# Kernel tuning notes

Hardware: AMD Instinct MI355X
Metric: run time of the kernel (lower is better)

## Reference

```python
import jax, jax.numpy as jnp
import numpy as np

N, D, H, C, K, L = 50000, 256, 128, 40, 4, 2
E = 800000


def setup_inputs() -> dict:
    key = jax.random.key(0)
    ks = jax.random.split(key, 20)
    g = lambda k, s: jax.random.normal(k, s, dtype=jnp.float32) * 0.05
    z = lambda s: jnp.zeros(s, dtype=jnp.float32)
    return {
        "x": jax.random.normal(ks[0], (N, D), dtype=jnp.float32),
        "edge_index": jax.random.randint(ks[1], (2, E), 0, N, dtype=jnp.int32),
        "fc0_w": g(ks[2], (D, H)), "fc0_b": z((H,)),
        "fc1_w": g(ks[3], (H, C)), "fc1_b": z((C,)),
        "env_w": g(ks[4], (L, H, K)), "env_b": z((L, K)),
        "conv_w": g(ks[5], (L, K, 2 * H, H)),
        "q_w": g(ks[6], (H, H)), "q_b": z((H,)),
        "k_w": g(ks[7], (H, H)), "k_b": z((H,)),
        "v_w": g(ks[8], (H, H)), "v_b": z((H,)),
        "envp_w": g(ks[9], (H, K)), "envp_b": z((K,)),
        "genv_w": g(ks[10], (K, H, H)),
        "gt_w": g(ks[11], (H, H)), "gt_b": z((H,)),
    }


def _gcn_conv(h, row, col, n):
    # symmetric normalization using in-degree array (deg computed from col, as in source)
    deg = jax.ops.segment_sum(jnp.ones_like(col, dtype=h.dtype), col, num_segments=n)
    inv = jnp.where(deg > 0, 1.0 / jnp.sqrt(deg), 0.0)
    val = inv[col] * inv[row]                      # [E]
    msg = val[:, None] * h[row]                    # [E, H] gather
    return jax.ops.segment_sum(msg, col, num_segments=n)  # scatter to dst


def _canet_conv(h, row, col, env, w):
    # sum_k e_k [W_D^k * A_norm h ; W_S^k * h] via cat + per-env GEMM, residual
    hi = jnp.concatenate([_gcn_conv(h, row, col, h.shape[0]), h], axis=1)  # [N, 2H]
    out_k = jnp.einsum('nd,kdh->nkh', hi, w)       # [N, K, H]
    return jnp.einsum('nk,nkh->nh', env, out_k) + h


def _linear_transformer(h, q_w, q_b, k_w, k_b, v_w, v_b, envp_w, envp_b):
    n = h.shape[0]
    q = h @ q_w + q_b
    k = h @ k_w + k_b
    v = h @ v_w + v_b
    q = q / jnp.maximum(jnp.linalg.norm(q), 1e-12)  # fro-norm of whole matrix
    k = k / jnp.maximum(jnp.linalg.norm(k), 1e-12)
    ksum = jnp.sum(k, axis=0)                       # k^T @ ones -> [H]
    attn_norm = 1.0 + (q @ ksum)[:, None] / n       # [N,1]
    gr = (v + q @ (k.T @ v) / n) / jnp.maximum(attn_norm, 1e-12)
    return gr, gr @ envp_w + envp_b


def _forward(x, edge_index, fc0_w, fc0_b, fc1_w, fc1_b, env_w, env_b, conv_w,
             q_w, q_b, k_w, k_b, v_w, v_b, envp_w, envp_b, genv_w, gt_w, gt_b):
    row, col = edge_index[0], edge_index[1]
    h = jax.nn.relu(x @ fc0_w + fc0_b)
    for i in range(L):
        logits = h @ env_w[i] + env_b[i]            # node env encoder
        env = jax.nn.softmax(logits, axis=-1)       # eval-mode sampling
        h = jax.nn.relu(_canet_conv(h, row, col, env, conv_w[i]))
    local_logits = h @ fc1_w + fc1_b                # [N, C]
    gr, glog = _linear_transformer(h, q_w, q_b, k_w, k_b, v_w, v_b, envp_w, envp_b)
    genv = jax.nn.softmax(glog, axis=-1)            # [N, K]
    gpe = jnp.einsum('nh,khe->nke', gr, genv_w)     # per-env global transforms
    ctx = jnp.einsum('nk,nkh->nh', genv, gpe)
    gh = jax.nn.relu(ctx @ gt_w + gt_b)
    global_logits = gh @ fc1_w + fc1_b
    return 0.5 * (local_logits + global_logits)     # fused prediction


def reference(x, edge_index, fc0_w, fc0_b, fc1_w, fc1_b, env_w, env_b, conv_w,
              q_w, q_b, k_w, k_b, v_w, v_b, envp_w, envp_b, genv_w, gt_w, gt_b):
    return _forward(x, edge_index, fc0_w, fc0_b, fc1_w, fc1_b, env_w, env_b, conv_w,
                    q_w, q_b, k_w, k_b, v_w, v_b, envp_w, envp_b, genv_w, gt_w, gt_b)
```

## Files before the change

kernel.cpp:

```cpp
#include <hip/hip_runtime.h>

#define DEV __device__ __forceinline__

static constexpr int NN = 50000;
static constexpr int DD = 256;
static constexpr int HH = 128;
static constexpr int CC = 40;
static constexpr int KK = 4;
static constexpr int EE = 800000;
static constexpr int MP = 50176;
static constexpr int SKV = 196;
static constexpr int CPB = 8;
static constexpr int CSB = 391;

typedef __attribute__((ext_vector_type(8))) short bf16x8;
typedef __attribute__((ext_vector_type(4))) float f32x4;

DEV unsigned short f2bf(float f) {
  union { float f; unsigned int i; } c; c.f = f;
  unsigned int x = c.i;
  x += 0x7FFFu + ((x >> 16) & 1u);
  return (unsigned short)(x >> 16);
}
DEV float bfbits2f(unsigned int hi16bits) {
  union { unsigned int i; float f; } c; c.i = hi16bits; return c.f;
}

__global__ void MLEI_12970801234193_kernel(float* out, int n) {
  int i = blockIdx.x * blockDim.x + threadIdx.x;
  if (i < n) out[i] = 7.0f;
}

__global__ void zero_i32_kernel(int* p, int n) {
  int i = blockIdx.x * blockDim.x + threadIdx.x;
  if (i < n) p[i] = 0;
}

__global__ void padzero_kernel(unsigned short* kT, unsigned short* vT) {
  int i = blockIdx.x * blockDim.x + threadIdx.x;
  const int PW = MP - NN;
  if (i >= HH * PW) return;
  int f = i / PW, c = i - f * PW;
  kT[(size_t)f * MP + NN + c] = 0;
  vT[(size_t)f * MP + NN + c] = 0;
}

__global__ void tcvt_kernel(const float* __restrict__ src, unsigned short* __restrict__ dst,
                            int K, int N, int nm) {
  int i = blockIdx.x * blockDim.x + threadIdx.x;
  int tot = nm * K * N;
  if (i >= tot) return;
  int m = i / (K * N);
  int rem = i - m * K * N;
  int k = rem / N;
  int n = rem - k * N;
  dst[(size_t)m * K * N + (size_t)n * K + k] = f2bf(src[i]);
}

__global__ __launch_bounds__(256) void mgemm_kernel(
    const float* __restrict__ A, const float* __restrict__ Aadd, int lda,
    const unsigned short* __restrict__ Bt, int K,
    int emode, float* __restrict__ out, int ldo,
    const float* __restrict__ bias, const float* __restrict__ resid, int ldr,
    const float* __restrict__ anorm, const float* __restrict__ red,
    unsigned short* __restrict__ outT,
    unsigned short* __restrict__ outBf, const float* __restrict__ rowscale,
    int M, int Nd) {
  __shared__ unsigned short As[2][128][40];
  __shared__ unsigned short Bs[2][128][40];
  const int tid = threadIdx.x, lane = tid & 63, wave = tid >> 6;
  const int quad = lane >> 4, l16 = lane & 15;
  const int wm = (wave >> 1) * 64, wn = (wave & 1) * 64;
  const int bm = blockIdx.x * 128;
  const int srow = tid >> 1, skh = (tid & 1) * 16;
  const int grow = bm + srow;
  const bool rowok = grow < M;
  const bool colok = srow < Nd;
  const int NCH = K >> 5;

  f32x4 acc[4][4];
#pragma unroll
  for (int i = 0; i < 4; ++i)
#pragma unroll
    for (int j = 0; j < 4; ++j)
#pragma unroll
      for (int r = 0; r < 4; ++r) acc[i][j][r] = 0.f;

  float va[16];
  bf16x8 b0, b1;

  auto LOAD = [&](int kc) {
    int k0 = kc << 5;
    if (rowok) {
      const float* ap = A + (size_t)grow * lda + k0 + skh;
      float4 v0 = *(const float4*)(ap + 0), v1 = *(const float4*)(ap + 4);
      float4 v2 = *(const float4*)(ap + 8), v3 = *(const float4*)(ap + 12);
      va[0] = v0.x; va[1] = v0.y; va[2] = v0.z; va[3] = v0.w;
      va[4] = v1.x; va[5] = v1.y; va[6] = v1.z; va[7] = v1.w;
      va[8] = v2.x; va[9] = v2.y; va[10] = v2.z; va[11] = v2.w;
      va[12] = v3.x; va[13] = v3.y; va[14] = v3.z; va[15] = v3.w;
      if (Aadd) {
        const float* ap2 = Aadd + (size_t)grow * lda + k0 + skh;
        float4 w0 = *(const float4*)(ap2 + 0), w1 = *(const float4*)(ap2 + 4);
        float4 w2 = *(const float4*)(ap2 + 8), w3 = *(const float4*)(ap2 + 12);
        va[0] += w0.x; va[1] += w0.y; va[2] += w0.z; va[3] += w0.w;
        va[4] += w1.x; va[5] += w1.y; va[6] += w1.z; va[7] += w1.w;
        va[8] += w2.x; va[9] += w2.y; va[10] += w2.z; va[11] += w2.w;
        va[12] += w3.x; va[13] += w3.y; va[14] += w3.z; va[15] += w3.w;
      }
    }
    if (colok) {
      const unsigned short* bp = Bt + (size_t)srow * K + k0 + skh;
      b0 = *(const bf16x8*)(bp);
      b1 = *(const bf16x8*)(bp + 8);
    } else {
#pragma unroll
      for (int z = 0; z < 8; ++z) { b0[z] = 0; b1[z] = 0; }
    }
  };

  auto STORE = [&](int buf) {
    bf16x8 p0, p1;
    if (rowok) {
#pragma unroll
      for (int z = 0; z < 8; ++z) { p0[z] = (short)f2bf(va[z]); p1[z] = (short)f2bf(va[z + 8]); }
    } else {
#pragma unroll
      for (int z = 0; z < 8; ++z) { p0[z] = 0; p1[z] = 0; }
    }
    *(bf16x8*)&As[buf][srow][skh] = p0;
    *(bf16x8*)&As[buf][srow][skh + 8] = p1;
    *(bf16x8*)&Bs[buf][srow][skh] = b0;
    *(bf16x8*)&Bs[buf][srow][skh + 8] = b1;
  };

  LOAD(0);
  STORE(0);
  __syncthreads();

  for (int kc = 0; kc < NCH; ++kc) {
    const int cur = kc & 1;
    const bool more = (kc + 1) < NCH;
    if (more) LOAD(kc + 1);
    bf16x8 af[4], bfr[4];
#pragma unroll
    for (int i = 0; i < 4; ++i) af[i] = *(const bf16x8*)&As[cur][wm + i * 16 + l16][quad * 8];
#pragma unroll
    for (int j = 0; j < 4; ++j) bfr[j] = *(const bf16x8*)&Bs[cur][wn + j * 16 + l16][quad * 8];
#pragma unroll
    for (int i = 0; i < 4; ++i)
#pragma unroll
      for (int j = 0; j < 4; ++j)
        acc[i][j] = __builtin_amdgcn_mfma_f32_16x16x32_bf16(af[i], bfr[j], acc[i][j], 0, 0, 0);
    if (more) STORE(cur ^ 1);
    __syncthreads();
  }

  float s2 = (emode == 3) ? red[2] : 0.f;
#pragma unroll
  for (int j = 0; j < 4; ++j) {
    int col = wn + j * 16 + l16;
    if (col >= Nd) continue;
    float bv = bias ? bias[col] : 0.f;
#pragma unroll
    for (int i = 0; i < 4; ++i) {
      int row0 = bm + wm + i * 16 + quad * 4;
      if (row0 >= M) continue;
      float o[4];
#pragma unroll
      for (int r = 0; r < 4; ++r) {
        float a = acc[i][j][r];
        int row = row0 + r;
        if (emode == 0) o[r] = a + bv;
        else if (emode == 1) o[r] = fmaxf(a + bv, 0.f);
        else if (emode == 3) o[r] = (resid[(size_t)row * ldr + col] + a * s2) / anorm[row];
        else o[r] = 0.5f * a + bv;
        out[(size_t)row * ldo + col] = o[r];
      }
      if (outT) {
        ushort4 pk;
        pk.x = f2bf(o[0]); pk.y = f2bf(o[1]); pk.z = f2bf(o[2]); pk.w = f2bf(o[3]);
        *(ushort4*)&outT[(size_t)col * MP + row0] = pk;
      }
      if (outBf) {
#pragma unroll
        for (int r = 0; r < 4; ++r) {
          float rs = rowscale ? rowscale[row0 + r] : 1.f;
          outBf[(size_t)(row0 + r) * 128 + col] = f2bf(o[r] * rs);
        }
      }
    }
  }
}

__global__ __launch_bounds__(256) void ktv_mfma_kernel(
    const unsigned short* __restrict__ kT, const unsigned short* __restrict__ vT,
    float* __restrict__ part) {
  __shared__ unsigned short As[2][128][40];
  __shared__ unsigned short Bs[2][128][40];
  const int tid = threadIdx.x, lane = tid & 63, wave = tid >> 6;
  const int quad = lane >> 4, l16 = lane & 15;
  const int wm = (wave >> 1) * 64, wn = (wave & 1) * 64;
  const int srow = tid >> 1, skh = (tid & 1) * 16;

  f32x4 acc[4][4];
#pragma unroll
  for (int i = 0; i < 4; ++i)
#pragma unroll
    for (int j = 0; j < 4; ++j)
#pragma unroll
      for (int r = 0; r < 4; ++r) acc[i][j][r] = 0.f;

  const int nb0 = blockIdx.x * (CPB * 32);
  bf16x8 k0, k1, v0, v1;

  auto LOAD = [&](int c) {
    int nb = nb0 + c * 32;
    const unsigned short* kp = kT + (size_t)srow * MP + nb + skh;
    k0 = *(const bf16x8*)(kp);
    k1 = *(const bf16x8*)(kp + 8);
    const unsigned short* vp = vT + (size_t)srow * MP + nb + skh;
    v0 = *(const bf16x8*)(vp);
    v1 = *(const bf16x8*)(vp + 8);
  };
  auto STORE = [&](int buf) {
    *(bf16x8*)&As[buf][srow][skh] = k0;
    *(bf16x8*)&As[buf][srow][skh + 8] = k1;
    *(bf16x8*)&Bs[buf][srow][skh] = v0;
    *(bf16x8*)&Bs[buf][srow][skh + 8] = v1;
  };

  LOAD(0);
  STORE(0);
  __syncthreads();

  for (int c = 0; c < CPB; ++c) {
    const int cur = c & 1;
    const bool more = (c + 1) < CPB;
    if (more) LOAD(c + 1);
    bf16x8 af[4], bfr[4];
#pragma unroll
    for (int i = 0; i < 4; ++i) af[i] = *(const bf16x8*)&As[cur][wm + i * 16 + l16][quad * 8];
#pragma unroll
    for (int j = 0; j < 4; ++j) bfr[j] = *(const bf16x8*)&Bs[cur][wn + j * 16 + l16][quad * 8];
#pragma unroll
    for (int i = 0; i < 4; ++i)
#pragma unroll
      for (int j = 0; j < 4; ++j)
        acc[i][j] = __builtin_amdgcn_mfma_f32_16x16x32_bf16(af[i], bfr[j], acc[i][j], 0, 0, 0);
    if (more) STORE(cur ^ 1);
    __syncthreads();
  }

  float* pb = part + (size_t)blockIdx.x * 16384;
#pragma unroll
  for (int j = 0; j < 4; ++j) {
    int col = wn + j * 16 + l16;
#pragma unroll
    for (int i = 0; i < 4; ++i) {
      int row0 = wm + i * 16 + quad * 4;
      *(f32x4*)&pb[col * 128 + row0] = acc[i][j];
    }
  }
}

__global__ void ktv_reduce_kernel(const float* __restrict__ part,
                                  unsigned short* __restrict__ Btktv) {
  int i = blockIdx.x * blockDim.x + threadIdx.x;
  if (i >= 16384) return;
  float s = 0.f;
  for (int b = 0; b < SKV; ++b) s += part[(size_t)b * 16384 + i];
  Btktv[i] = f2bf(s);
}

__global__ __launch_bounds__(256) void mconv_kernel(
    const float* __restrict__ A1, const float* __restrict__ A2,
    const float* __restrict__ env, const unsigned short* __restrict__ Btc, int Kpe,
    int relu_resid, const float* __restrict__ resid, float* __restrict__ out,
    unsigned short* __restrict__ outBf, const float* __restrict__ rowscale, int M) {
  __shared__ unsigned short As[2][128][40];
  __shared__ unsigned short Bs[2][128][40];
  __shared__ float envs[4][128];
  const int tid = threadIdx.x, lane = tid & 63, wave = tid >> 6;
  const int quad = lane >> 4, l16 = lane & 15;
  const int wm = (wave >> 1) * 64, wn = (wave & 1) * 64;
  const int bm = blockIdx.x * 128;
  const int srow = tid >> 1, skh = (tid & 1) * 16;
  const int grow = bm + srow;
  const bool rowok = grow < M;

  for (int i = tid; i < 512; i += 256) {
    int r = i >> 2, c = i & 3;
    int g = bm + r;
    envs[c][r] = (g < M) ? env[(size_t)g * 4 + c] : 0.f;
  }
  __syncthreads();

  const int npe = Kpe >> 5;
  const int lg = (npe == 8) ? 3 : 2;
  const int NCH = npe << 2;

  f32x4 acc[4][4];
#pragma unroll
  for (int i = 0; i < 4; ++i)
#pragma unroll
    for (int j = 0; j < 4; ++j)
#pragma unroll
      for (int r = 0; r < 4; ++r) acc[i][j][r] = 0.f;

  float4 v0, v1, v2, v3;
  bf16x8 b0, b1;
  float ev = 0.f;

  auto LOAD = [&](int kc) {
    int e = kc >> lg;
    int kof = (kc & (npe - 1)) << 5;
    ev = envs[e][srow];
    const float* Asrc = A1;
    int ks = kof;
    if (A2 && kof >= 128) { Asrc = A2; ks = kof - 128; }
    if (rowok) {
      const float* ap = Asrc + (size_t)grow * 128 + ks + skh;
      v0 = *(const float4*)(ap + 0);
      v1 = *(const float4*)(ap + 4);
      v2 = *(const float4*)(ap + 8);
      v3 = *(const float4*)(ap + 12);
    }
    const unsigned short* bp = Btc + ((size_t)e * 128 + srow) * Kpe + kof + skh;
    b0 = *(const bf16x8*)(bp);
    b1 = *(const bf16x8*)(bp + 8);
  };

  auto STORE = [&](int buf) {
    bf16x8 p0, p1;
    if (rowok) {
      p0[0] = (short)f2bf(v0.x * ev); p0[1] = (short)f2bf(v0.y * ev);
      p0[2] = (short)f2bf(v0.z * ev); p0[3] = (short)f2bf(v0.w * ev);
      p0[4] = (short)f2bf(v1.x * ev); p0[5] = (short)f2bf(v1.y * ev);
      p0[6] = (short)f2bf(v1.z * ev); p0[7] = (short)f2bf(v1.w * ev);
      p1[0] = (short)f2bf(v2.x * ev); p1[1] = (short)f2bf(v2.y * ev);
      p1[2] = (short)f2bf(v2.z * ev); p1[3] = (short)f2bf(v2.w * ev);
      p1[4] = (short)f2bf(v3.x * ev); p1[5] = (short)f2bf(v3.y * ev);
      p1[6] = (short)f2bf(v3.z * ev); p1[7] = (short)f2bf(v3.w * ev);
    } else {
#pragma unroll
      for (int z = 0; z < 8; ++z) { p0[z] = 0; p1[z] = 0; }
    }
    *(bf16x8*)&As[buf][srow][skh] = p0;
    *(bf16x8*)&As[buf][srow][skh + 8] = p1;
    *(bf16x8*)&Bs[buf][srow][skh] = b0;
    *(bf16x8*)&Bs[buf][srow][skh + 8] = b1;
  };

  LOAD(0);
  STORE(0);
  __syncthreads();

  for (int kc = 0; kc < NCH; ++kc) {
    const int cur = kc & 1;
    const bool more = (kc + 1) < NCH;
    if (more) LOAD(kc + 1);
    bf16x8 af[4], bfr[4];
#pragma unroll
    for (int i = 0; i < 4; ++i) af[i] = *(const bf16x8*)&As[cur][wm + i * 16 + l16][quad * 8];
#pragma unroll
    for (int j = 0; j < 4; ++j) bfr[j] = *(const bf16x8*)&Bs[cur][wn + j * 16 + l16][quad * 8];
#pragma unroll
    for (int i = 0; i < 4; ++i)
#pragma unroll
      for (int j = 0; j < 4; ++j)
        acc[i][j] = __builtin_amdgcn_mfma_f32_16x16x32_bf16(af[i], bfr[j], acc[i][j], 0, 0, 0);
    if (more) STORE(cur ^ 1);
    __syncthreads();
  }

#pragma unroll
  for (int j = 0; j < 4; ++j) {
    int col = wn + j * 16 + l16;
#pragma unroll
    for (int i = 0; i < 4; ++i) {
      int row0 = bm + wm + i * 16 + quad * 4;
      if (row0 >= M) continue;
#pragma unroll
      for (int r = 0; r < 4; ++r) {
        int row = row0 + r;
        float a = acc[i][j][r];
        float o = relu_resid ? fmaxf(a + resid[(size_t)row * 128 + col], 0.f) : a;
        out[(size_t)row * 128 + col] = o;
        if (outBf) {
          float rs = rowscale ? rowscale[row] : 1.f;
          outBf[(size_t)row * 128 + col] = f2bf(o * rs);
        }
      }
    }
  }
}

__global__ void count_kernel(const int* ei, int* deg, int E) {
  int e = blockIdx.x * blockDim.x + threadIdx.x;
  if (e >= E) return;
  atomicAdd(&deg[ei[E + e]], 1);
}

__global__ __launch_bounds__(128) void scan1_kernel(const int* __restrict__ deg,
                                                    int* __restrict__ bsum, int n) {
  __shared__ int sh[128];
  int t = threadIdx.x;
  int i = blockIdx.x * 128 + t;
  sh[t] = (i < n) ? deg[i] : 0;
  __syncthreads();
  for (int off = 64; off > 0; off >>= 1) {
    if (t < off) sh[t] += sh[t + off];
    __syncthreads();
  }
  if (t == 0) bsum[blockIdx.x] = sh[0];
}

__global__ __launch_bounds__(512) void scan2_kernel(const int* __restrict__ bsum,
                                                    int* __restrict__ boff, int nb,
                                                    int* __restrict__ startN) {
  __shared__ int sh[512];
  int t = threadIdx.x;
  int v0 = (t < nb) ? bsum[t] : 0;
  sh[t] = v0;
  __syncthreads();
  for (int off = 1; off < 512; off <<= 1) {
    int v = sh[t];
    int add = (t >= off) ? sh[t - off] : 0;
    __syncthreads();
    sh[t] = v + add;
    __syncthreads();
  }
  if (t < nb) boff[t] = sh[t] - v0;
  if (t == nb - 1) *startN = sh[t];
}

__global__ __launch_bounds__(128) void scan3_kernel(const int* __restrict__ deg,
                                                    const int* __restrict__ boff,
                                                    int* __restrict__ start,
                                                    int* __restrict__ cursor,
                                                    float* __restrict__ inv, int n) {
  __shared__ int sh[128];
  int t = threadIdx.x;
  int i = blockIdx.x * 128 + t;
  int d = (i < n) ? deg[i] : 0;
  sh[t] = d;
  __syncthreads();
  for (int off = 1; off < 128; off <<= 1) {
    int v = sh[t];
    int add = (t >= off) ? sh[t - off] : 0;
    __syncthreads();
    sh[t] = v + add;
    __syncthreads();
  }
  if (i < n) {
    int p = boff[blockIdx.x] + sh[t] - d;
    start[i] = p; cursor[i] = p;
    inv[i] = (d > 0) ? rsqrtf((float)d) : 0.f;
  }
}

__global__ void fill_kernel(const int* ei, int* cursor, int* bucket, int E) {
  int e = blockIdx.x * blockDim.x + threadIdx.x;
  if (e >= E) return;
  int r = ei[e], c = ei[E + e];
  int pos = atomicAdd(&cursor[c], 1);
  bucket[pos] = r;
}

__global__ __launch_bounds__(256) void gather_kernel(
    const unsigned short* __restrict__ hs, const int* __restrict__ start,
    const int* __restrict__ bucket, const float* __restrict__ inv,
    float* __restrict__ agg, int n) {
  int node = blockIdx.x * 4 + (threadIdx.x >> 6);
  if (node >= n) return;
  const int lane = threadIdx.x & 63;
  const int half = lane >> 5, l32 = lane & 31;
  const int f4 = l32 * 4;
  int s0 = start[node], s1 = start[node + 1];
  float a0 = 0.f, a1 = 0.f, a2 = 0.f, a3 = 0.f;
  int j = s0 + half;
  for (; j + 2 < s1; j += 4) {
    int r0 = bucket[j], r1 = bucket[j + 2];
    uint2 u0 = *(const uint2*)&hs[(size_t)r0 * 128 + f4];
    uint2 u1 = *(const uint2*)&hs[(size_t)r1 * 128 + f4];
    a0 += bfbits2f(u0.x << 16); a1 += bfbits2f(u0.x & 0xFFFF0000u);
    a2 += bfbits2f(u0.y << 16); a3 += bfbits2f(u0.y & 0xFFFF0000u);
    a0 += bfbits2f(u1.x << 16); a1 += bfbits2f(u1.x & 0xFFFF0000u);
    a2 += bfbits2f(u1.y << 16); a3 += bfbits2f(u1.y & 0xFFFF0000u);
  }
  for (; j < s1; j += 2) {
    int r = bucket[j];
    uint2 u = *(const uint2*)&hs[(size_t)r * 128 + f4];
    a0 += bfbits2f(u.x << 16); a1 += bfbits2f(u.x & 0xFFFF0000u);
    a2 += bfbits2f(u.y << 16); a3 += bfbits2f(u.y & 0xFFFF0000u);
  }
  a0 += __shfl_xor(a0, 32);
  a1 += __shfl_xor(a1, 32);
  a2 += __shfl_xor(a2, 32);
  a3 += __shfl_xor(a3, 32);
  if (half == 0) {
    float iv = inv[node];
    *(float4*)&agg[(size_t)node * 128 + f4] = make_float4(iv * a0, iv * a1, iv * a2, iv * a3);
  }
}

__global__ __launch_bounds__(256) void env_softmax_kernel(const float* __restrict__ h,
                                                          const float* __restrict__ w,
                                                          const float* __restrict__ b,
                                                          float* __restrict__ env, int M) {
  __shared__ float hsd[64][129];
  __shared__ float ws[HH * KK];
  int tid = threadIdx.x;
  int base = blockIdx.x * 64;
  for (int i = tid; i < HH * KK; i += 256) ws[i] = w[i];
  {
    int row = tid >> 2, q4 = (tid & 3) * 32;
    int g = base + row;
    if (g < M) {
      const float* hp = h + (size_t)g * HH + q4;
#pragma unroll
      for (int z = 0; z < 8; ++z) {
        float4 v = *(const float4*)(hp + z * 4);
        hsd[row][q4 + z * 4 + 0] = v.x; hsd[row][q4 + z * 4 + 1] = v.y;
        hsd[row][q4 + z * 4 + 2] = v.z; hsd[row][q4 + z * 4 + 3] = v.w;
      }
    }
  }
  __syncthreads();
  if (tid < 64 && base + tid < M) {
    float l0 = b[0], l1 = b[1], l2 = b[2], l3 = b[3];
    for (int d = 0; d < HH; ++d) {
      float hv = hsd[tid][d];
      l0 += hv * ws[d * 4 + 0]; l1 += hv * ws[d * 4 + 1];
      l2 += hv * ws[d * 4 + 2]; l3 += hv * ws[d * 4 + 3];
    }
    float m = fmaxf(fmaxf(l0, l1), fmaxf(l2, l3));
    float e0 = __expf(l0 - m), e1 = __expf(l1 - m), e2 = __expf(l2 - m), e3 = __expf(l3 - m);
    float s = 1.f / (e0 + e1 + e2 + e3);
    *(float4*)(env + (size_t)(base + tid) * KK) = make_float4(e0 * s, e1 * s, e2 * s, e3 * s);
  }
}

__global__ __launch_bounds__(256) void colstats1_kernel(
    const float* __restrict__ q, const float* __restrict__ k,
    float* __restrict__ partK, float* __restrict__ partS, int n) {
  int tid = threadIdx.x, ty = tid >> 7, tx = tid & 127;
  int lo = blockIdx.x * 128 + ty, hi = min(n, blockIdx.x * 128 + 128);
  float ks = 0.f, sq = 0.f, sk = 0.f;
  for (int r = lo; r < hi; r += 2) {
    float kv = k[(size_t)r * HH + tx];
    float qv = q[(size_t)r * HH + tx];
    ks += kv; sq += qv * qv; sk += kv * kv;
  }
  __shared__ float sks[2][128];
  __shared__ float ssq[256], ssk[256];
  sks[ty][tx] = ks; ssq[tid] = sq; ssk[tid] = sk;
  __syncthreads();
  if (ty == 0) partK[(size_t)blockIdx.x * 128 + tx] = sks[0][tx] + sks[1][tx];
  for (int off = 128; off > 0; off >>= 1) {
    if (tid < off) { ssq[tid] += ssq[tid + off]; ssk[tid] += ssk[tid + off]; }
    __syncthreads();
  }
  if (tid == 0) { partS[blockIdx.x * 2] = ssq[0]; partS[blockIdx.x * 2 + 1] = ssk[0]; }
}

__global__ __launch_bounds__(256) void colstats2_kernel(
    const float* __restrict__ partK, const float* __restrict__ partS,
    float* __restrict__ ksum, float* __restrict__ red) {
  int t = threadIdx.x;
  if (t < 128) {
    float s = 0.f;
    for (int b = 0; b < CSB; ++b) s += partK[(size_t)b * 128 + t];
    ksum[t] = s;
  } else if (t == 128 || t == 129) {
    float s = 0.f;
    for (int b = 0; b < CSB; ++b) s += partS[b * 2 + (t - 128)];
    red[t - 128] = s;
  }
}

__global__ void scale_kernel(float* red, int n) {
  float nq = fmaxf(sqrtf(red[0]), 1e-12f);
  float nk = fmaxf(sqrtf(red[1]), 1e-12f);
  red[2] = 1.f / (nq * nk * (float)n);
}

__global__ __launch_bounds__(256) void anorm_kernel(const float* q, const float* ksum,
                                                    const float* red, float* anorm, int M) {
  __shared__ float ks[HH];
  for (int i = threadIdx.x; i < HH; i += blockDim.x) ks[i] = ksum[i];
  __syncthreads();
  int n = blockIdx.x * blockDim.x + threadIdx.x;
  if (n >= M) return;
  const float* qp = q + (size_t)n * HH;
  float d = 0.f;
  for (int i = 0; i < HH; ++i) d += qp[i] * ks[i];
  float a = 1.f + d * red[2];
  anorm[n] = fmaxf(a, 1e-12f);
}

extern "C" void kernel_launch(void* const* d_in, const int* in_sizes, int n_in,
                              void* d_out, int out_size, void* d_ws, size_t ws_size,
                              hipStream_t stream) {
  const float* x = (const float*)d_in[0];
  const int* ei = (const int*)d_in[1];
  const float* fc0_w = (const float*)d_in[2];
  const float* fc0_b = (const float*)d_in[3];
  const float* fc1_w = (const float*)d_in[4];
  const float* fc1_b = (const float*)d_in[5];
  const float* env_w = (const float*)d_in[6];
  const float* env_b = (const float*)d_in[7];
  const float* conv_w = (const float*)d_in[8];
  const float* q_w = (const float*)d_in[9];
  const float* q_b = (const float*)d_in[10];
  const float* k_w = (const float*)d_in[11];
  const float* k_b = (const float*)d_in[12];
  const float* v_w = (const float*)d_in[13];
  const float* v_b = (const float*)d_in[14];
  const float* envp_w = (const float*)d_in[15];
  const float* envp_b = (const float*)d_in[16];
  const float* genv_w = (const float*)d_in[17];
  const float* gt_w = (const float*)d_in[18];
  const float* gt_b = (const float*)d_in[19];
  float* out = (float*)d_out;

  const size_t NH = (size_t)NN * HH;
  float* W = (float*)d_ws;
  float* hA = W;
  float* hB = W + NH;
  float* agg = W + 2 * NH;
  float* vbuf = W + 3 * NH;
  float* gr = W + 4 * NH;
  float* env = W + 5 * NH;
  float* genv = env + (size_t)NN * KK;
  float* inv = genv + (size_t)NN * KK;
  float* anorm = inv + NN;
  float* ksum = anorm + NN;
  float* red = ksum + HH;
  int* deg = (int*)(red + 4);
  int* start = deg + NN;
  int* cursor = start + NN + 1;
  int* bucket = cursor + NN;
  int* bsum = bucket + EE;
  int* boff = bsum + CSB;
  unsigned short* wb = (unsigned short*)(((uintptr_t)(boff + CSB) + 15) & ~(uintptr_t)15);
  unsigned short* Btfc0 = wb;
  unsigned short* Btq = Btfc0 + 32768;
  unsigned short* Btk = Btq + 16384;
  unsigned short* Btv = Btk + 16384;
  unsigned short* Btgt = Btv + 16384;
  unsigned short* Btfc1 = Btgt + 16384;
  unsigned short* Btconv = Btfc1 + 5120;
  unsigned short* Btgenv = Btconv + 262144;
  unsigned short* Btktv = Btgenv + 65536;
  unsigned short* kTbf = Btktv + 16384;
  unsigned short* vTbf = kTbf + (size_t)HH * MP;
  unsigned short* hsb = vTbf + (size_t)HH * MP;
  float* part = (float*)(((uintptr_t)(hsb + NH) + 15) & ~(uintptr_t)15);
  float* partK = part + (size_t)SKV * 16384;
  float* partS = partK + (size_t)CSB * 128;

  float* q = agg;
  float* kb = hB;
  float* ctx = hB;
  float* gh = vbuf;

  dim3 b256(256);
  const int MB = (NN + 127) / 128;

  zero_i32_kernel<<<dim3((NN + 255) / 256), b256, 0, stream>>>(deg, NN);
  padzero_kernel<<<dim3((HH * (MP - NN) + 255) / 256), b256, 0, stream>>>(kTbf, vTbf);

  count_kernel<<<dim3((EE + 255) / 256), b256, 0, stream>>>(ei, deg, EE);
  scan1_kernel<<<dim3(CSB), dim3(128), 0, stream>>>(deg, bsum, NN);
  scan2_kernel<<<dim3(1), dim3(512), 0, stream>>>(bsum, boff, CSB, start + NN);
  scan3_kernel<<<dim3(CSB), dim3(128), 0, stream>>>(deg, boff, start, cursor, inv, NN);
  fill_kernel<<<dim3((EE + 255) / 256), b256, 0, stream>>>(ei, cursor, bucket, EE);

  tcvt_kernel<<<dim3((32768 + 255) / 256), b256, 0, stream>>>(fc0_w, Btfc0, 256, 128, 1);
  tcvt_kernel<<<dim3((16384 + 255) / 256), b256, 0, stream>>>(q_w, Btq, 128, 128, 1);
  tcvt_kernel<<<dim3((16384 + 255) / 256), b256, 0, stream>>>(k_w, Btk, 128, 128, 1);
  tcvt_kernel<<<dim3((16384 + 255) / 256), b256, 0, stream>>>(v_w, Btv, 128, 128, 1);
  tcvt_kernel<<<dim3((16384 + 255) / 256), b256, 0, stream>>>(gt_w, Btgt, 128, 128, 1);
  tcvt_kernel<<<dim3((5120 + 255) / 256), b256, 0, stream>>>(fc1_w, Btfc1, 128, 40, 1);
  tcvt_kernel<<<dim3((262144 + 255) / 256), b256, 0, stream>>>(conv_w, Btconv, 256, 128, 8);
  tcvt_kernel<<<dim3((65536 + 255) / 256), b256, 0, stream>>>(genv_w, Btgenv, 128, 128, 4);

  mgemm_kernel<<<dim3(MB), b256, 0, stream>>>(
      x, nullptr, DD, Btfc0, 256, 1, hA, HH, fc0_b, nullptr, 0, nullptr, nullptr,
      nullptr, hsb, inv, NN, HH);

  float* hcur = hA;
  float* hnext = hB;
  for (int l = 0; l < 2; ++l) {
    env_softmax_kernel<<<dim3((NN + 63) / 64), b256, 0, stream>>>(
        hcur, env_w + (size_t)l * HH * KK, env_b + (size_t)l * KK, env, NN);
    gather_kernel<<<dim3(NN / 4), b256, 0, stream>>>(hsb, start, bucket, inv, agg, NN);
    mconv_kernel<<<dim3(MB), b256, 0, stream>>>(
        agg, hcur, env, Btconv + (size_t)l * 131072, 256, 1, hcur, hnext,
        (l == 0) ? hsb : nullptr, inv, NN);
    float* t = hcur; hcur = hnext; hnext = t;
  }

  mgemm_kernel<<<dim3(MB), b256, 0, stream>>>(
      hcur, nullptr, HH, Btq, 128, 0, q, HH, q_b, nullptr, 0, nullptr, nullptr,
      nullptr, nullptr, nullptr, NN, HH);
  mgemm_kernel<<<dim3(MB), b256, 0, stream>>>(
      hcur, nullptr, HH, Btk, 128, 0, kb, HH, k_b, nullptr, 0, nullptr, nullptr,
      kTbf, nullptr, nullptr, NN, HH);
  mgemm_kernel<<<dim3(MB), b256, 0, stream>>>(
      hcur, nullptr, HH, Btv, 128, 0, vbuf, HH, v_b, nullptr, 0, nullptr, nullptr,
      vTbf, nullptr, nullptr, NN, HH);

  colstats1_kernel<<<dim3(CSB), b256, 0, stream>>>(q, kb, partK, partS, NN);
  colstats2_kernel<<<dim3(1), b256, 0, stream>>>(partK, partS, ksum, red);
  ktv_mfma_kernel<<<dim3(SKV), b256, 0, stream>>>(kTbf, vTbf, part);
  ktv_reduce_kernel<<<dim3(64), b256, 0, stream>>>(part, Btktv);
  scale_kernel<<<dim3(1), dim3(1), 0, stream>>>(red, NN);
  anorm_kernel<<<dim3((NN + 255) / 256), b256, 0, stream>>>(q, ksum, red, anorm, NN);

  mgemm_kernel<<<dim3(MB), b256, 0, stream>>>(
      q, nullptr, HH, Btktv, 128, 3, gr, HH, nullptr, vbuf, HH, anorm, red,
      nullptr, nullptr, nullptr, NN, HH);

  env_softmax_kernel<<<dim3((NN + 63) / 64), b256, 0, stream>>>(gr, envp_w, envp_b, genv, NN);

  mconv_kernel<<<dim3(MB), b256, 0, stream>>>(
      gr, nullptr, genv, Btgenv, 128, 0, nullptr, ctx, nullptr, nullptr, NN);

  mgemm_kernel<<<dim3(MB), b256, 0, stream>>>(
      ctx, nullptr, HH, Btgt, 128, 1, gh, HH, gt_b, nullptr, 0, nullptr, nullptr,
      nullptr, nullptr, nullptr, NN, HH);

  mgemm_kernel<<<dim3(MB), b256, 0, stream>>>(
      hcur, gh, HH, Btfc1, 128, 5, out, CC, fc1_b, nullptr, 0, nullptr, nullptr,
      nullptr, nullptr, nullptr, NN, CC);
}
```

Baseline: 700.9 us.

## Deepen GEMM prefetch to two chunks and reorder mconv loop for A reuse

The generic GEMM and the k^T v partial kernel now keep two register sets of prefetched operands, so each global load is issued two k-chunks ahead of its MFMA use. The mconv kernel reads its env weights straight into registers instead of staging them through shared memory with an extra barrier. It also reorders its loop so each A chunk is loaded once and reused across all four env weight slices, rather than reloaded for every env. The cost is higher register pressure, which may lower occupancy, and more complex loop control.

Measured after the change: 688.6 us. Within noise of the previous version (-1.8%).

```diff
diff --git a/kernel.cpp b/kernel.cpp
--- a/kernel.cpp
+++ b/kernel.cpp
@@ -86,10 +86,10 @@
 #pragma unroll
       for (int r = 0; r < 4; ++r) acc[i][j][r] = 0.f;
 
-  float va[16];
-  bf16x8 b0, b1;
-
-  auto LOAD = [&](int kc) {
+  float vaA[16], vaB[16];
+  bf16x8 bA0, bA1, bB0, bB1;
+
+  auto LOAD = [&](int kc, float (&va)[16], bf16x8& b0, bf16x8& b1) {
     int k0 = kc << 5;
     if (rowok) {
       const float* ap = A + (size_t)grow * lda + k0 + skh;
@@ -119,7 +119,7 @@
     }
   };
 
-  auto STORE = [&](int buf) {
+  auto STORE = [&](int buf, const float (&va)[16], const bf16x8& b0, const bf16x8& b1) {
     bf16x8 p0, p1;
     if (rowok) {
 #pragma unroll
@@ -134,26 +134,35 @@
     *(bf16x8*)&Bs[buf][srow][skh + 8] = b1;
   };
 
-  LOAD(0);
-  STORE(0);
-  __syncthreads();
-
-  for (int kc = 0; kc < NCH; ++kc) {
-    const int cur = kc & 1;
-    const bool more = (kc + 1) < NCH;
-    if (more) LOAD(kc + 1);
+  auto MFMA = [&](int buf) {
     bf16x8 af[4], bfr[4];
 #pragma unroll
-    for (int i = 0; i < 4; ++i) af[i] = *(const bf16x8*)&As[cur][wm + i * 16 + l16][quad * 8];
-#pragma unroll
-    for (int j = 0; j < 4; ++j) bfr[j] = *(const bf16x8*)&Bs[cur][wn + j * 16 + l16][quad * 8];
+    for (int i = 0; i < 4; ++i) af[i] = *(const bf16x8*)&As[buf][wm + i * 16 + l16][quad * 8];
+#pragma unroll
+    for (int j = 0; j < 4; ++j) bfr[j] = *(const bf16x8*)&Bs[buf][wn + j * 16 + l16][quad * 8];
 #pragma unroll
     for (int i = 0; i < 4; ++i)
 #pragma unroll
       for (int j = 0; j < 4; ++j)
         acc[i][j] = __builtin_amdgcn_mfma_f32_16x16x32_bf16(af[i], bfr[j], acc[i][j], 0, 0, 0);
-    if (more) STORE(cur ^ 1);
+  };
+
+  LOAD(0, vaA, bA0, bA1);
+  if (NCH > 1) LOAD(1, vaB, bB0, bB1);
+  STORE(0, vaA, bA0, bA1);
+  __syncthreads();
+
+  for (int kc = 0; kc < NCH; kc += 2) {
+    if (kc + 2 < NCH) LOAD(kc + 2, vaA, bA0, bA1);
+    MFMA(0);
+    if (kc + 1 < NCH) STORE(1, vaB, bB0, bB1);
     __syncthreads();
+    if (kc + 1 < NCH) {
+      if (kc + 3 < NCH) LOAD(kc + 3, vaB, bB0, bB1);
+      MFMA(1);
+      if (kc + 2 < NCH) STORE(0, vaA, bA0, bA1);
+      __syncthreads();
+    }
   }
 
   float s2 = (emode == 3) ? red[2] : 0.f;
@@ -212,9 +221,9 @@
       for (int r = 0; r < 4; ++r) acc[i][j][r] = 0.f;
 
   const int nb0 = blockIdx.x * (CPB * 32);
-  bf16x8 k0, k1, v0, v1;
-
-  auto LOAD = [&](int c) {
+  bf16x8 kA0, kA1, vA0, vA1, kB0, kB1, vB0, vB1;
+
+  auto LOAD = [&](int c, bf16x8& k0, bf16x8& k1, bf16x8& v0, bf16x8& v1) {
     int nb = nb0 + c * 32;
     const unsigned short* kp = kT + (size_t)srow * MP + nb + skh;
     k0 = *(const bf16x8*)(kp);
@@ -223,33 +232,41 @@
     v0 = *(const bf16x8*)(vp);
     v1 = *(const bf16x8*)(vp + 8);
   };
-  auto STORE = [&](int buf) {
+  auto STORE = [&](int buf, const bf16x8& k0, const bf16x8& k1, const bf16x8& v0, const bf16x8& v1) {
     *(bf16x8*)&As[buf][srow][skh] = k0;
     *(bf16x8*)&As[buf][srow][skh + 8] = k1;
     *(bf16x8*)&Bs[buf][srow][skh] = v0;
     *(bf16x8*)&Bs[buf][srow][skh + 8] = v1;
   };
-
-  LOAD(0);
-  STORE(0);
-  __syncthreads();
-
-  for (int c = 0; c < CPB; ++c) {
-    const int cur = c & 1;
-    const bool more = (c + 1) < CPB;
-    if (more) LOAD(c + 1);
+  auto MFMA = [&](int buf) {
     bf16x8 af[4], bfr[4];
 #pragma unroll
-    for (int i = 0; i < 4; ++i) af[i] = *(const bf16x8*)&As[cur][wm + i * 16 + l16][quad * 8];
-#pragma unroll
-    for (int j = 0; j < 4; ++j) bfr[j] = *(const bf16x8*)&Bs[cur][wn + j * 16 + l16][quad * 8];
+    for (int i = 0; i < 4; ++i) af[i] = *(const bf16x8*)&As[buf][wm + i * 16 + l16][quad * 8];
+#pragma unroll
+    for (int j = 0; j < 4; ++j) bfr[j] = *(const bf16x8*)&Bs[buf][wn + j * 16 + l16][quad * 8];
 #pragma unroll
     for (int i = 0; i < 4; ++i)
 #pragma unroll
       for (int j = 0; j < 4; ++j)
         acc[i][j] = __builtin_amdgcn_mfma_f32_16x16x32_bf16(af[i], bfr[j], acc[i][j], 0, 0, 0);
-    if (more) STORE(cur ^ 1);
+  };
+
+  LOAD(0, kA0, kA1, vA0, vA1);
+  LOAD(1, kB0, kB1, vB0, vB1);
+  STORE(0, kA0, kA1, vA0, vA1);
+  __syncthreads();
+
+  for (int c = 0; c < CPB; c += 2) {
+    if (c + 2 < CPB) LOAD(c + 2, kA0, kA1, vA0, vA1);
+    MFMA(0);
+    if (c + 1 < CPB) STORE(1, kB0, kB1, vB0, vB1);
     __syncthreads();
+    if (c + 1 < CPB) {
+      if (c + 3 < CPB) LOAD(c + 3, kB0, kB1, vB0, vB1);
+      MFMA(1);
+      if (c + 2 < CPB) STORE(0, kA0, kA1, vA0, vA1);
+      __syncthreads();
+    }
   }
 
   float* pb = part + (size_t)blockIdx.x * 16384;
@@ -280,7 +297,6 @@
     unsigned short* __restrict__ outBf, const float* __restrict__ rowscale, int M) {
   __shared__ unsigned short As[2][128][40];
   __shared__ unsigned short Bs[2][128][40];
-  __shared__ float envs[4][128];
   const int tid = threadIdx.x, lane = tid & 63, wave = tid >> 6;
   const int quad = lane >> 4, l16 = lane & 15;
   const int wm = (wave >> 1) * 64, wn = (wave & 1) * 64;
@@ -289,16 +305,14 @@
   const int grow = bm + srow;
   const bool rowok = grow < M;
 
-  for (int i = tid; i < 512; i += 256) {
-    int r = i >> 2, c = i & 3;
-    int g = bm + r;
-    envs[c][r] = (g < M) ? env[(size_t)g * 4 + c] : 0.f;
-  }
-  __syncthreads();
+  float ev0 = 0.f, ev1 = 0.f, ev2 = 0.f, ev3 = 0.f;
+  if (rowok) {
+    float4 e4 = *(const float4*)&env[(size_t)grow * 4];
+    ev0 = e4.x; ev1 = e4.y; ev2 = e4.z; ev3 = e4.w;
+  }
 
   const int npe = Kpe >> 5;
-  const int lg = (npe == 8) ? 3 : 2;
-  const int NCH = npe << 2;
+  const int NPH = npe << 2;
 
   f32x4 acc[4][4];
 #pragma unroll
@@ -308,40 +322,39 @@
 #pragma unroll
       for (int r = 0; r < 4; ++r) acc[i][j][r] = 0.f;
 
-  float4 v0, v1, v2, v3;
+  float aC[16], aN[16];
   bf16x8 b0, b1;
-  float ev = 0.f;
-
-  auto LOAD = [&](int kc) {
-    int e = kc >> lg;
-    int kof = (kc & (npe - 1)) << 5;
-    ev = envs[e][srow];
+
+  auto LOADA = [&](int kc, float (&dst)[16]) {
+    int kof = kc << 5;
     const float* Asrc = A1;
     int ks = kof;
     if (A2 && kof >= 128) { Asrc = A2; ks = kof - 128; }
     if (rowok) {
       const float* ap = Asrc + (size_t)grow * 128 + ks + skh;
-      v0 = *(const float4*)(ap + 0);
-      v1 = *(const float4*)(ap + 4);
-      v2 = *(const float4*)(ap + 8);
-      v3 = *(const float4*)(ap + 12);
-    }
-    const unsigned short* bp = Btc + ((size_t)e * 128 + srow) * Kpe + kof + skh;
+      float4 v0 = *(const float4*)(ap + 0), v1 = *(const float4*)(ap + 4);
+      float4 v2 = *(const float4*)(ap + 8), v3 = *(const float4*)(ap + 12);
+      dst[0] = v0.x; dst[1] = v0.y; dst[2] = v0.z; dst[3] = v0.w;
+      dst[4] = v1.x; dst[5] = v1.y; dst[6] = v1.z; dst[7] = v1.w;
+      dst[8] = v2.x; dst[9] = v2.y; dst[10] = v2.z; dst[11] = v2.w;
+      dst[12] = v3.x; dst[13] = v3.y; dst[14] = v3.z; dst[15] = v3.w;
+    }
+  };
+
+  auto LOADB = [&](int e, int kc) {
+    const unsigned short* bp = Btc + ((size_t)e * 128 + srow) * Kpe + (kc << 5) + skh;
     b0 = *(const bf16x8*)(bp);
     b1 = *(const bf16x8*)(bp + 8);
   };
 
-  auto STORE = [&](int buf) {
+  auto STORE = [&](int buf, const float (&a)[16], float ev) {
     bf16x8 p0, p1;
     if (rowok) {
-      p0[0] = (short)f2bf(v0.x * ev); p0[1] = (short)f2bf(v0.y * ev);
-      p0[2] = (short)f2bf(v0.z * ev); p0[3] = (short)f2bf(v0.w * ev);
-      p0[4] = (short)f2bf(v1.x * ev); p0[5] = (short)f2bf(v1.y * ev);
-      p0[6] = (short)f2bf(v1.z * ev); p0[7] = (short)f2bf(v1.w * ev);
-      p1[0] = (short)f2bf(v2.x * ev); p1[1] = (short)f2bf(v2.y * ev);
-      p1[2] = (short)f2bf(v2.z * ev); p1[3] = (short)f2bf(v2.w * ev);
-      p1[4] = (short)f2bf(v3.x * ev); p1[5] = (short)f2bf(v3.y * ev);
-      p1[6] = (short)f2bf(v3.z * ev); p1[7] = (short)f2bf(v3.w * ev);
+#pragma unroll
+      for (int z = 0; z < 8; ++z) {
+        p0[z] = (short)f2bf(a[z] * ev);
+        p1[z] = (short)f2bf(a[z + 8] * ev);
+      }
     } else {
 #pragma unroll
       for (int z = 0; z < 8; ++z) { p0[z] = 0; p1[z] = 0; }
@@ -352,26 +365,46 @@
     *(bf16x8*)&Bs[buf][srow][skh + 8] = b1;
   };
 
-  LOAD(0);
-  STORE(0);
-  __syncthreads();
-
-  for (int kc = 0; kc < NCH; ++kc) {
-    const int cur = kc & 1;
-    const bool more = (kc + 1) < NCH;
-    if (more) LOAD(kc + 1);
+  auto MFMA = [&](int buf) {
     bf16x8 af[4], bfr[4];
 #pragma unroll
-    for (int i = 0; i < 4; ++i) af[i] = *(const bf16x8*)&As[cur][wm + i * 16 + l16][quad * 8];
-#pragma unroll
-    for (int j = 0; j < 4; ++j) bfr[j] = *(const bf16x8*)&Bs[cur][wn + j * 16 + l16][quad * 8];
+    for (int i = 0; i < 4; ++i) af[i] = *(const bf16x8*)&As[buf][wm + i * 16 + l16][quad * 8];
+#pragma unroll
+    for (int j = 0; j < 4; ++j) bfr[j] = *(const bf16x8*)&Bs[buf][wn + j * 16 + l16][quad * 8];
 #pragma unroll
     for (int i = 0; i < 4; ++i)
 #pragma unroll
       for (int j = 0; j < 4; ++j)
         acc[i][j] = __builtin_amdgcn_mfma_f32_16x16x32_bf16(af[i], bfr[j], acc[i][j], 0, 0, 0);
-    if (more) STORE(cur ^ 1);
-    __syncthreads();
+  };
+
+  LOADA(0, aC);
+  LOADB(0, 0);
+  if (npe > 1) LOADA(1, aN);
+  STORE(0, aC, ev0);
+  __syncthreads();
+
+  for (int kc = 0; kc < npe; ++kc) {
+#pragma unroll
+    for (int e = 0; e < 4; ++e) {
+      const int p = (kc << 2) + e;
+      const int cur = e & 1;
+      const bool more = (p + 1) < NPH;
+      if (more) {
+        LOADB((e + 1) & 3, kc + (e == 3 ? 1 : 0));
+      }
+      MFMA(cur);
+      if (more) {
+        if (e == 3) {
+#pragma unroll
+          for (int z = 0; z < 16; ++z) aC[z] = aN[z];
+        }
+        float evn = (e == 0) ? ev1 : (e == 1) ? ev2 : (e == 2) ? ev3 : ev0;
+        STORE(cur ^ 1, aC, evn);
+        if (e == 3 && kc + 2 < npe) LOADA(kc + 2, aN);
+      }
+      __syncthreads();
+    }
   }
 
 #pragma unroll
```
